# Performance work log

Measured on AMD Instinct MI355X. Metric: run time of the kernel, lower is better.

Reference implementation:

```python
import jax, jax.numpy as jnp
import numpy as np

B, D, H, C = 8192, 2048, 4096, 64
HALF = D // 2
BLOCKS = 2


def setup_inputs() -> dict:
    key = jax.random.key(0)
    ks = jax.random.split(key, 8)
    z = jax.random.normal(ks[0], (B, D), jnp.float32)
    condition = jax.random.normal(ks[1], (B, C), jnp.float32)
    # alternating masks: block 0 identity=odd indices, transform=even; block 1 flipped
    even = jnp.arange(0, D, 2, dtype=jnp.int32)
    odd = jnp.arange(1, D, 2, dtype=jnp.int32)
    idx_id = jnp.stack([odd, even])   # [BLOCKS, HALF]
    idx_tr = jnp.stack([even, odd])   # [BLOCKS, HALF]
    def init_w(k, shape, fan_in):
        return jax.random.normal(k, shape, jnp.float32) * np.float32(1.0 / np.sqrt(fan_in))
    W1 = init_w(ks[2], (BLOCKS, HALF + C, H), HALF + C)
    b1 = jnp.zeros((BLOCKS, H), jnp.float32)
    W2 = init_w(ks[3], (BLOCKS, H, H), H)
    b2 = jnp.zeros((BLOCKS, H), jnp.float32)
    W3 = init_w(ks[4], (BLOCKS, H, 2 * HALF), H) * np.float32(0.01)  # keep exp(S) tame
    b3 = jnp.zeros((BLOCKS, 2 * HALF), jnp.float32)
    return {"z": z, "condition": condition, "idx_id": idx_id, "idx_tr": idx_tr,
            "W1": W1, "b1": b1, "W2": W2, "b2": b2, "W3": W3, "b3": b3}


def reference(z, condition, idx_id, idx_tr, W1, b1, W2, b2, W3, b3):
    # F_zx of the affine coupling layer (scale_tanh=False, clamp_scale=None)
    x = z
    log_det = jnp.zeros((z.shape[0], 1), z.dtype)
    for i in range(BLOCKS):
        # gather identity channels, condition on external vector
        h = jnp.concatenate([x[:, idx_id[i]], condition], axis=-1)  # [B, HALF+C]
        h = jax.nn.relu(h @ W1[i] + b1[i])
        h = jax.nn.relu(h @ W2[i] + b2[i])
        out = (h @ W3[i] + b3[i]).reshape(x.shape[0], HALF, 2)
        S = out[..., 0]  # scale logits
        T = out[..., 1]  # translation
        # scatter-update transformed channels
        x = x.at[:, idx_tr[i]].set(x[:, idx_tr[i]] * jnp.exp(S) + T)
        log_det = log_det + jnp.sum(S, axis=1, keepdims=True)
    return x, log_det
```

## Files before the change

### kernel.cpp

```cpp
#include <hip/hip_runtime.h>
#include <hip/hip_bf16.h>

#define B_    8192
#define D_    2048
#define H_    4096
#define C_    64
#define HALF_ 1024
#define KIN_  1088

typedef __attribute__((ext_vector_type(8))) short bf16x8;
typedef __attribute__((ext_vector_type(4))) float f32x4;

__device__ __forceinline__ unsigned short f2bf(float f) {
  __hip_bfloat16 h = __float2bfloat16(f);
  return *reinterpret_cast<unsigned short*>(&h);
}

__device__ __forceinline__ void gload16(const void* g, void* s) {
  __builtin_amdgcn_global_load_lds((const __attribute__((address_space(1))) void*)g,
                                   (__attribute__((address_space(3))) void*)s,
                                   16, 0, 0);
}

__global__ void convT(const float* __restrict__ W, unsigned short* __restrict__ Wt,
                      int K, int N) {
  __shared__ float tile[32][33];
  int tx = threadIdx.x & 31, ty = threadIdx.x >> 5;
  int n0 = blockIdx.x * 32, k0 = blockIdx.y * 32;
#pragma unroll
  for (int i = 0; i < 4; ++i)
    tile[ty + i * 8][tx] = W[(size_t)(k0 + ty + i * 8) * N + n0 + tx];
  __syncthreads();
#pragma unroll
  for (int i = 0; i < 4; ++i)
    Wt[(size_t)(n0 + ty + i * 8) * K + k0 + tx] = f2bf(tile[tx][ty + i * 8]);
}

__global__ void build_act(const float* __restrict__ x, const float* __restrict__ cond,
                          const int* __restrict__ idx_id, unsigned short* __restrict__ A0) {
  int row = blockIdx.y;
  int col = blockIdx.x * 256 + threadIdx.x;
  if (col >= KIN_) return;
  float v = (col < HALF_) ? x[(size_t)row * D_ + idx_id[col]]
                          : cond[(size_t)row * C_ + (col - HALF_)];
  A0[(size_t)row * KIN_ + col] = f2bf(v);
}

template <int RELU, int OUTF32>
__global__ __launch_bounds__(512, 2)
void gemm8p(const unsigned short* __restrict__ A,
            const unsigned short* __restrict__ Bt,
            const float* __restrict__ bias,
            void* __restrict__ Cout,
            int M, int N, int K) {
  __shared__ unsigned short lds[65536];
  char* ldsb = (char*)lds;
  const int tid = threadIdx.x;
  const int w = tid >> 6, lane = tid & 63;
  const int fr = lane & 15, fq = lane >> 4;
  const int wr = w >> 2, wc = w & 3;

  const int nbx = N >> 8;
  const int nwg = (int)gridDim.x;
  const int cpx = nwg >> 3;
  const int bid = (int)blockIdx.x;
  const int swz = (bid & 7) * cpx + (bid >> 3);
  const int by = swz / nbx, bx = swz - by * nbx;
  const int m0 = by << 8, n0 = bx << 8;

  const int chunkp = (((fr & 1) << 2) | fq) ^ (fr >> 1);
  const int A0 = (wr * 64 + (fr >> 1)) * 128 + chunkp * 16;
  const int B0 = 32768 + (wc * 32 + (fr >> 1)) * 128 + chunkp * 16;

  int rS[2], kcolS[2];
#pragma unroll
  for (int s = 0; s < 2; ++s) {
    int q = s * 512 + w * 64 + lane;
    int p = q >> 3, cph = q & 7;
    int clg = cph ^ (p & 7);
    rS[s] = 2 * p + (clg >> 2);
    kcolS[s] = (clg & 3) * 8;
  }
  const unsigned short* sA0 = A + (size_t)(m0 + rS[0]) * K + kcolS[0];
  const unsigned short* sA1 = A + (size_t)(m0 + rS[1]) * K + kcolS[1];
  const unsigned short* sB0 = Bt + (size_t)(n0 + rS[0]) * K + kcolS[0];
  const unsigned short* sB1 = Bt + (size_t)(n0 + rS[1]) * K + kcolS[1];
  const int dst0 = w * 1024 + lane * 16;

#define STAGE_A(KK, TILE, BUF) do {                                          \
    gload16(sA0 + (TILE) * 64 + (KK) * 32,                                   \
            ldsb + (BUF) + (KK) * 16384 + dst0);                             \
    gload16(sA1 + (TILE) * 64 + (KK) * 32,                                   \
            ldsb + (BUF) + (KK) * 16384 + 8192 + dst0);                      \
  } while (0)
#define STAGE_B(KK, TILE, BUF) do {                                          \
    gload16(sB0 + (TILE) * 64 + (KK) * 32,                                   \
            ldsb + (BUF) + 32768 + (KK) * 16384 + dst0);                     \
    gload16(sB1 + (TILE) * 64 + (KK) * 32,                                   \
            ldsb + (BUF) + 32768 + (KK) * 16384 + 8192 + dst0);              \
  } while (0)

  f32x4 acc[8][4];
  f32x4 z4 = {0.f, 0.f, 0.f, 0.f};
#pragma unroll
  for (int m = 0; m < 8; ++m)
#pragma unroll
    for (int n = 0; n < 4; ++n) acc[m][n] = z4;

  const int NT = K >> 6;

  STAGE_A(0, 0, 0);
  STAGE_A(1, 0, 0);
  STAGE_B(0, 0, 0);
  STAGE_B(1, 0, 0);
  STAGE_B(0, 1, 65536);
  STAGE_A(0, 1, 65536);
  STAGE_B(1, 1, 65536);
  asm volatile("s_waitcnt vmcnt(6)" ::: "memory");
  __builtin_amdgcn_sched_barrier(0);
  __builtin_amdgcn_s_barrier();

#define PHASE_TAIL()                                                         \
    __builtin_amdgcn_sched_barrier(0);                                       \
    __builtin_amdgcn_s_barrier();                                            \
    asm volatile("s_waitcnt lgkmcnt(0)" ::: "memory");                       \
    __builtin_amdgcn_sched_barrier(0);

#define TILE8(TT, S1, S234, DO_VM)                                           \
  {                                                                          \
    const int bufC = ((TT) & 1) * 65536;                                     \
    const int bufN = 65536 - bufC;                                           \
    bf16x8 av[4], bv[4];                                                     \
                               \
    _Pragma("unroll") for (int m = 0; m < 4; ++m)                            \
      av[m] = *(const bf16x8*)(ldsb + bufC + A0 + m * 1024);                 \
    _Pragma("unroll") for (int n = 0; n < 4; ++n)                            \
      bv[n] = *(const bf16x8*)(ldsb + bufC + B0 + n * 1024);                 \
    if (S1) { STAGE_A(1, (TT) + 1, bufN); }                                  \
    PHASE_TAIL()                                                             \
    __builtin_amdgcn_s_setprio(1);                                           \
    _Pragma("unroll") for (int m = 0; m < 4; ++m)                            \
      _Pragma("unroll") for (int n = 0; n < 4; ++n)                          \
        acc[m][n] = __builtin_amdgcn_mfma_f32_16x16x32_bf16(av[m], bv[n],    \
                                                        acc[m][n], 0, 0, 0); \
    __builtin_amdgcn_s_setprio(0);                                           \
    __builtin_amdgcn_sched_barrier(0);                                       \
    __builtin_amdgcn_s_barrier();                                            \
                                 \
    _Pragma("unroll") for (int m = 0; m < 4; ++m)                            \
      av[m] = *(const bf16x8*)(ldsb + bufC + A0 + (m + 4) * 1024);           \
    if (S234) { STAGE_B(0, (TT) + 2, bufC); }                                \
    PHASE_TAIL()                                                             \
    __builtin_amdgcn_s_setprio(1);                                           \
    _Pragma("unroll") for (int m = 0; m < 4; ++m)                            \
      _Pragma("unroll") for (int n = 0; n < 4; ++n)                          \
        acc[m + 4][n] = __builtin_amdgcn_mfma_f32_16x16x32_bf16(av[m], bv[n],\
                                                    acc[m + 4][n], 0, 0, 0); \
    __builtin_amdgcn_s_setprio(0);                                           \
    __builtin_amdgcn_sched_barrier(0);                                       \
    __builtin_amdgcn_s_barrier();                                            \
                               \
    _Pragma("unroll") for (int m = 0; m < 4; ++m)                            \
      av[m] = *(const bf16x8*)(ldsb + bufC + A0 + m * 1024 + 16384);         \
    _Pragma("unroll") for (int n = 0; n < 4; ++n)                            \
      bv[n] = *(const bf16x8*)(ldsb + bufC + B0 + n * 1024 + 16384);         \
    if (S234) { STAGE_A(0, (TT) + 2, bufC); }                                \
    PHASE_TAIL()                                                             \
    __builtin_amdgcn_s_setprio(1);                                           \
    _Pragma("unroll") for (int m = 0; m < 4; ++m)                            \
      _Pragma("unroll") for (int n = 0; n < 4; ++n)                          \
        acc[m][n] = __builtin_amdgcn_mfma_f32_16x16x32_bf16(av[m], bv[n],    \
                                                        acc[m][n], 0, 0, 0); \
    __builtin_amdgcn_s_setprio(0);                                           \
    __builtin_amdgcn_sched_barrier(0);                                       \
    __builtin_amdgcn_s_barrier();                                            \
                                           \
    _Pragma("unroll") for (int m = 0; m < 4; ++m)                            \
      av[m] = *(const bf16x8*)(ldsb + bufC + A0 + (m + 4) * 1024 + 16384);   \
    if (S234) { STAGE_B(1, (TT) + 2, bufC); }                                \
    PHASE_TAIL()                                                             \
    __builtin_amdgcn_s_setprio(1);                                           \
    _Pragma("unroll") for (int m = 0; m < 4; ++m)                            \
      _Pragma("unroll") for (int n = 0; n < 4; ++n)                          \
        acc[m + 4][n] = __builtin_amdgcn_mfma_f32_16x16x32_bf16(av[m], bv[n],\
                                                    acc[m + 4][n], 0, 0, 0); \
    __builtin_amdgcn_s_setprio(0);                                           \
    __builtin_amdgcn_sched_barrier(0);                                       \
    if (DO_VM == 1) asm volatile("s_waitcnt vmcnt(6)" ::: "memory");         \
    if (DO_VM == 2) asm volatile("s_waitcnt vmcnt(0)" ::: "memory");         \
    __builtin_amdgcn_sched_barrier(0);                                       \
    __builtin_amdgcn_s_barrier();                                            \
  }

  for (int T = 0; T < NT - 2; ++T) {
    TILE8(T, 1, 1, 1)
  }
  TILE8(NT - 2, 1, 0, 2)
  TILE8(NT - 1, 0, 0, 0)
#undef TILE8
#undef PHASE_TAIL
#undef STAGE_A
#undef STAGE_B

#pragma unroll
  for (int n = 0; n < 4; ++n) {
    int gcol = n0 + wc * 64 + n * 16 + fr;
    float bb = bias[gcol];
#pragma unroll
    for (int m = 0; m < 8; ++m) {
      int grow = m0 + wr * 128 + m * 16 + fq * 4;
#pragma unroll
      for (int r = 0; r < 4; ++r) {
        float v = acc[m][n][r] + bb;
        if (RELU) v = fmaxf(v, 0.f);
        if (OUTF32)
          ((float*)Cout)[(size_t)(grow + r) * N + gcol] = v;
        else
          ((unsigned short*)Cout)[(size_t)(grow + r) * N + gcol] = f2bf(v);
      }
    }
  }
}

__global__ void update_kernel(float* __restrict__ x, float* __restrict__ logdet,
                              const float* __restrict__ ST, const int* __restrict__ idx_tr) {
  int row = blockIdx.x;
  int tid = threadIdx.x;
  const float2* st = (const float2*)(ST + (size_t)row * D_);
  float* xr = x + (size_t)row * D_;
  float ssum = 0.f;
  for (int j = tid; j < HALF_; j += 256) {
    float2 v = st[j];
    int c = idx_tr[j];
    xr[c] = xr[c] * expf(v.x) + v.y;
    ssum += v.x;
  }
  ssum += __shfl_down(ssum, 32);
  ssum += __shfl_down(ssum, 16);
  ssum += __shfl_down(ssum, 8);
  ssum += __shfl_down(ssum, 4);
  ssum += __shfl_down(ssum, 2);
  ssum += __shfl_down(ssum, 1);
  __shared__ float wsum[4];
  if ((tid & 63) == 0) wsum[tid >> 6] = ssum;
  __syncthreads();
  if (tid == 0) logdet[row] += wsum[0] + wsum[1] + wsum[2] + wsum[3];
}

extern "C" void kernel_launch(void* const* d_in, const int* in_sizes, int n_in,
                              void* d_out, int out_size, void* d_ws, size_t ws_size,
                              hipStream_t stream) {
  const float* z    = (const float*)d_in[0];
  const float* cond = (const float*)d_in[1];
  const int* idx_id = (const int*)d_in[2];
  const int* idx_tr = (const int*)d_in[3];
  const float* W1   = (const float*)d_in[4];
  const float* b1   = (const float*)d_in[5];
  const float* W2   = (const float*)d_in[6];
  const float* b2   = (const float*)d_in[7];
  const float* W3   = (const float*)d_in[8];
  const float* b3   = (const float*)d_in[9];

  float* xout   = (float*)d_out;
  float* logdet = xout + (size_t)B_ * D_;

  char* ws = (char*)d_ws;
  unsigned short* Wt = (unsigned short*)ws;
  unsigned short* H1 = (unsigned short*)(ws + 33554432);
  unsigned short* H2 = (unsigned short*)(ws + 33554432 + 67108864);
  float* ST = (float*)H1;
  unsigned short* A0 = H2;

  hipMemcpyAsync(xout, z, (size_t)B_ * D_ * sizeof(float), hipMemcpyDeviceToDevice, stream);
  hipMemsetAsync(logdet, 0, B_ * sizeof(float), stream);

  for (int blk = 0; blk < 2; ++blk) {
    const float* W1b = W1 + (size_t)blk * KIN_ * H_;
    const float* W2b = W2 + (size_t)blk * H_ * H_;
    const float* W3b = W3 + (size_t)blk * H_ * D_;
    const float* b1b = b1 + (size_t)blk * H_;
    const float* b2b = b2 + (size_t)blk * H_;
    const float* b3b = b3 + (size_t)blk * D_;
    const int* idi = idx_id + blk * HALF_;
    const int* idt = idx_tr + blk * HALF_;

    convT<<<dim3(H_ / 32, KIN_ / 32), 256, 0, stream>>>(W1b, Wt, KIN_, H_);
    build_act<<<dim3(5, B_), 256, 0, stream>>>(xout, cond, idi, A0);
    gemm8p<1, 0><<<dim3((H_ / 256) * (B_ / 256)), 512, 0, stream>>>(A0, Wt, b1b, H1, B_, H_, KIN_);

    convT<<<dim3(H_ / 32, H_ / 32), 256, 0, stream>>>(W2b, Wt, H_, H_);
    gemm8p<1, 0><<<dim3((H_ / 256) * (B_ / 256)), 512, 0, stream>>>(H1, Wt, b2b, H2, B_, H_, H_);

    convT<<<dim3(D_ / 32, H_ / 32), 256, 0, stream>>>(W3b, Wt, H_, D_);
    gemm8p<0, 1><<<dim3((D_ / 256) * (B_ / 256)), 512, 0, stream>>>(H2, Wt, b3b, ST, B_, D_, H_);

    update_kernel<<<dim3(B_), 256, 0, stream>>>(xout, logdet, ST, idt);
  }
}
```

Before: 1.057 ms.

## Fuse coupling update into last GEMM epilogue and stage bf16 stores via LDS

```diff
diff --git a/kernel.cpp b/kernel.cpp
--- a/kernel.cpp
+++ b/kernel.cpp
@@ -36,22 +36,24 @@
     Wt[(size_t)(n0 + ty + i * 8) * K + k0 + tx] = f2bf(tile[tx][ty + i * 8]);
 }
 
-__global__ void build_act(const float* __restrict__ x, const float* __restrict__ cond,
-                          const int* __restrict__ idx_id, unsigned short* __restrict__ A0) {
+__global__ void build_act(const float* __restrict__ xsrc, const float* __restrict__ cond,
+                          int par, unsigned short* __restrict__ A0) {
   int row = blockIdx.y;
   int col = blockIdx.x * 256 + threadIdx.x;
   if (col >= KIN_) return;
-  float v = (col < HALF_) ? x[(size_t)row * D_ + idx_id[col]]
+  float v = (col < HALF_) ? xsrc[(size_t)row * D_ + col * 2 + par]
                           : cond[(size_t)row * C_ + (col - HALF_)];
   A0[(size_t)row * KIN_ + col] = f2bf(v);
 }
 
-template <int RELU, int OUTF32>
+template <int MODE>
 __global__ __launch_bounds__(512, 2)
 void gemm8p(const unsigned short* __restrict__ A,
             const unsigned short* __restrict__ Bt,
             const float* __restrict__ bias,
-            void* __restrict__ Cout,
+            unsigned short* __restrict__ Cout,
+            const float* __restrict__ xold, float* __restrict__ xnew,
+            float* __restrict__ part, int par,
             int M, int N, int K) {
   __shared__ unsigned short lds[65536];
   char* ldsb = (char*)lds;
@@ -202,49 +204,72 @@
 #undef STAGE_A
 #undef STAGE_B
 
-#pragma unroll
-  for (int n = 0; n < 4; ++n) {
-    int gcol = n0 + wc * 64 + n * 16 + fr;
-    float bb = bias[gcol];
+  if (MODE == 0) {
+#pragma unroll
+    for (int m = 0; m < 8; ++m)
+#pragma unroll
+      for (int n = 0; n < 4; ++n) {
+        int gcol = n0 + wc * 64 + n * 16 + fr;
+        float bb = bias[gcol];
+#pragma unroll
+        for (int r = 0; r < 4; ++r) {
+          float v = fmaxf(acc[m][n][r] + bb, 0.f);
+          int lrow = m * 16 + fq * 4 + r;
+          *(unsigned short*)(ldsb + w * 16384 + lrow * 128 + ((n ^ fq) * 32) + fr * 2) = f2bf(v);
+        }
+      }
+    asm volatile("s_waitcnt lgkmcnt(0)" ::: "memory");
+    __builtin_amdgcn_sched_barrier(0);
+    unsigned short* Cb = Cout + (size_t)(m0 + wr * 128) * N + n0 + wc * 64;
+    const int sub = lane & 7;
+#pragma unroll
+    for (int i = 0; i < 16; ++i) {
+      int lrow = i * 8 + (lane >> 3);
+      int phys = (sub >> 1) ^ ((lrow >> 2) & 3);
+      bf16x8 val = *(const bf16x8*)(ldsb + w * 16384 + lrow * 128 + phys * 32 + (sub & 1) * 16);
+      *(bf16x8*)(Cb + (size_t)lrow * N + sub * 8) = val;
+    }
+  } else {
 #pragma unroll
     for (int m = 0; m < 8; ++m) {
-      int grow = m0 + wr * 128 + m * 16 + fq * 4;
+      float srow[4] = {0.f, 0.f, 0.f, 0.f};
+#pragma unroll
+      for (int n = 0; n < 4; ++n) {
+        int gcol = n0 + wc * 64 + n * 16 + fr;
+        float bb = bias[gcol];
+#pragma unroll
+        for (int r = 0; r < 4; ++r) {
+          float v = acc[m][n][r] + bb;
+          float vp = __shfl_xor(v, 1);
+          if (!(fr & 1)) {
+            int grow = m0 + wr * 128 + m * 16 + fq * 4 + r;
+            float xo = xold[(size_t)grow * N + gcol + par];
+            xnew[(size_t)grow * N + gcol + par] = xo * expf(v) + vp;
+            srow[r] += v;
+          }
+        }
+      }
 #pragma unroll
       for (int r = 0; r < 4; ++r) {
-        float v = acc[m][n][r] + bb;
-        if (RELU) v = fmaxf(v, 0.f);
-        if (OUTF32)
-          ((float*)Cout)[(size_t)(grow + r) * N + gcol] = v;
-        else
-          ((unsigned short*)Cout)[(size_t)(grow + r) * N + gcol] = f2bf(v);
+        float s = srow[r];
+        s += __shfl_xor(s, 2);
+        s += __shfl_xor(s, 4);
+        s += __shfl_xor(s, 8);
+        if (fr == 0) {
+          int grow = m0 + wr * 128 + m * 16 + fq * 4 + r;
+          part[(size_t)grow * 32 + bx * 4 + wc] = s;
+        }
       }
     }
   }
 }
 
-__global__ void update_kernel(float* __restrict__ x, float* __restrict__ logdet,
-                              const float* __restrict__ ST, const int* __restrict__ idx_tr) {
-  int row = blockIdx.x;
-  int tid = threadIdx.x;
-  const float2* st = (const float2*)(ST + (size_t)row * D_);
-  float* xr = x + (size_t)row * D_;
-  float ssum = 0.f;
-  for (int j = tid; j < HALF_; j += 256) {
-    float2 v = st[j];
-    int c = idx_tr[j];
-    xr[c] = xr[c] * expf(v.x) + v.y;
-    ssum += v.x;
-  }
-  ssum += __shfl_down(ssum, 32);
-  ssum += __shfl_down(ssum, 16);
-  ssum += __shfl_down(ssum, 8);
-  ssum += __shfl_down(ssum, 4);
-  ssum += __shfl_down(ssum, 2);
-  ssum += __shfl_down(ssum, 1);
-  __shared__ float wsum[4];
-  if ((tid & 63) == 0) wsum[tid >> 6] = ssum;
-  __syncthreads();
-  if (tid == 0) logdet[row] += wsum[0] + wsum[1] + wsum[2] + wsum[3];
+__global__ void reduce_logdet(const float* __restrict__ P, float* __restrict__ logdet, int add) {
+  int row = blockIdx.x * 256 + threadIdx.x;
+  float s = 0.f;
+#pragma unroll
+  for (int g = 0; g < 32; ++g) s += P[(size_t)row * 32 + g];
+  logdet[row] = add ? (logdet[row] + s) : s;
 }
 
 extern "C" void kernel_launch(void* const* d_in, const int* in_sizes, int n_in,
@@ -252,8 +277,6 @@
                               hipStream_t stream) {
   const float* z    = (const float*)d_in[0];
   const float* cond = (const float*)d_in[1];
-  const int* idx_id = (const int*)d_in[2];
-  const int* idx_tr = (const int*)d_in[3];
   const float* W1   = (const float*)d_in[4];
   const float* b1   = (const float*)d_in[5];
   const float* W2   = (const float*)d_in[6];
@@ -268,11 +291,8 @@
   unsigned short* Wt = (unsigned short*)ws;
   unsigned short* H1 = (unsigned short*)(ws + 33554432);
   unsigned short* H2 = (unsigned short*)(ws + 33554432 + 67108864);
-  float* ST = (float*)H1;
+  float* Pp = (float*)H1;
   unsigned short* A0 = H2;
-
-  hipMemcpyAsync(xout, z, (size_t)B_ * D_ * sizeof(float), hipMemcpyDeviceToDevice, stream);
-  hipMemsetAsync(logdet, 0, B_ * sizeof(float), stream);
 
   for (int blk = 0; blk < 2; ++blk) {
     const float* W1b = W1 + (size_t)blk * KIN_ * H_;
@@ -281,19 +301,21 @@
     const float* b1b = b1 + (size_t)blk * H_;
     const float* b2b = b2 + (size_t)blk * H_;
     const float* b3b = b3 + (size_t)blk * D_;
-    const int* idi = idx_id + blk * HALF_;
-    const int* idt = idx_tr + blk * HALF_;
+    const float* xsrc = blk ? xout : z;
 
     convT<<<dim3(H_ / 32, KIN_ / 32), 256, 0, stream>>>(W1b, Wt, KIN_, H_);
-    build_act<<<dim3(5, B_), 256, 0, stream>>>(xout, cond, idi, A0);
-    gemm8p<1, 0><<<dim3((H_ / 256) * (B_ / 256)), 512, 0, stream>>>(A0, Wt, b1b, H1, B_, H_, KIN_);
+    build_act<<<dim3(5, B_), 256, 0, stream>>>(xsrc, cond, 1 - blk, A0);
+    gemm8p<0><<<dim3((H_ / 256) * (B_ / 256)), 512, 0, stream>>>(
+        A0, Wt, b1b, H1, nullptr, nullptr, nullptr, 0, B_, H_, KIN_);
 
     convT<<<dim3(H_ / 32, H_ / 32), 256, 0, stream>>>(W2b, Wt, H_, H_);
-    gemm8p<1, 0><<<dim3((H_ / 256) * (B_ / 256)), 512, 0, stream>>>(H1, Wt, b2b, H2, B_, H_, H_);
+    gemm8p<0><<<dim3((H_ / 256) * (B_ / 256)), 512, 0, stream>>>(
+        H1, Wt, b2b, H2, nullptr, nullptr, nullptr, 0, B_, H_, H_);
 
     convT<<<dim3(D_ / 32, H_ / 32), 256, 0, stream>>>(W3b, Wt, H_, D_);
-    gemm8p<0, 1><<<dim3((D_ / 256) * (B_ / 256)), 512, 0, stream>>>(H2, Wt, b3b, ST, B_, D_, H_);
-
-    update_kernel<<<dim3(B_), 256, 0, stream>>>(xout, logdet, ST, idt);
-  }
-}
+    gemm8p<1><<<dim3((D_ / 256) * (B_ / 256)), 512, 0, stream>>>(
+        H2, Wt, b3b, nullptr, z, xout, Pp, blk, B_, D_, H_);
+
+    reduce_logdet<<<dim3(B_ / 256), 256, 0, stream>>>(Pp, logdet, blk);
+  }
+}
```

Result: no change. 1.050 ms (-0.7%).
